# Kernel tuning notes

Measured on AMD Instinct MI355X. Metric: run time of the kernel, lower is better.

## Reference

```python
import jax, jax.numpy as jnp
import numpy as np

NUM_HEADS = 8
NUM_KV_HEADS = 2
HEAD_DIM = 64
EPS = 1e-6
ROPE_BASE = 10000.0


def rmsnorm(x, w):
    # x: (..., head_dim)
    var = jnp.mean(x * x, axis=-1, keepdims=True)
    return x * jax.lax.rsqrt(var + EPS) * w


def apply_rope(x):
    # x: (B, L, nH, hd); positions along L, standard rotate-half RoPE
    B, L, nH, hd = x.shape
    inv_freq = 1.0 / (ROPE_BASE ** (jnp.arange(0, hd, 2, dtype=jnp.float32) / hd))  # (hd/2,)
    ang = jnp.arange(L, dtype=jnp.float32)[:, None] * inv_freq[None, :]  # (L, hd/2)
    cos = jnp.concatenate([jnp.cos(ang), jnp.cos(ang)], axis=-1)[None, :, None, :]  # (1,L,1,hd)
    sin = jnp.concatenate([jnp.sin(ang), jnp.sin(ang)], axis=-1)[None, :, None, :]
    x1, x2 = jnp.split(x, 2, axis=-1)
    rot = jnp.concatenate([-x2, x1], axis=-1)
    return x * cos + rot * sin


def setup_inputs() -> dict:
    key = jax.random.key(0)
    ks = jax.random.split(key, 6)
    width = 512
    x = jax.random.normal(ks[0], (1, 16, 16, 16, width), dtype=jnp.float32)
    s = 1.0 / np.sqrt(width)
    Wq = jax.random.normal(ks[1], (width, width), dtype=jnp.float32) * s
    Wk = jax.random.normal(ks[2], (NUM_KV_HEADS * HEAD_DIM, width), dtype=jnp.float32) * s
    Wv = jax.random.normal(ks[3], (NUM_KV_HEADS * HEAD_DIM, width), dtype=jnp.float32) * s
    Wo = jax.random.normal(ks[4], (width, width), dtype=jnp.float32) * s
    q_norm_w = jnp.ones((HEAD_DIM,), dtype=jnp.float32)
    k_norm_w = jnp.ones((HEAD_DIM,), dtype=jnp.float32)
    return {"x": x, "Wq": Wq, "Wk": Wk, "Wv": Wv,
            "q_norm_w": q_norm_w, "k_norm_w": k_norm_w, "Wo": Wo}


def reference(x, Wq, Wk, Wv, q_norm_w, k_norm_w, Wo):
    B, H, W, D, C = x.shape
    L = H * W * D
    xf = x.reshape(B, L, C)
    q = (xf @ Wq.T).reshape(B, L, NUM_HEADS, HEAD_DIM)
    k = (xf @ Wk.T).reshape(B, L, NUM_KV_HEADS, HEAD_DIM)
    v = (xf @ Wv.T).reshape(B, L, NUM_KV_HEADS, HEAD_DIM)
    q = apply_rope(rmsnorm(q, q_norm_w))
    k = apply_rope(rmsnorm(k, k_norm_w))
    # (B, heads, L, hd)
    q = q.transpose(0, 2, 1, 3)
    k = k.transpose(0, 2, 1, 3)
    v = v.transpose(0, 2, 1, 3)
    repeats = NUM_HEADS // NUM_KV_HEADS
    if repeats > 1:
        k = jnp.repeat(k, repeats, axis=1)
        v = jnp.repeat(v, repeats, axis=1)
    scale = 1.0 / np.sqrt(HEAD_DIM)
    scores = jnp.einsum('bhqd,bhkd->bhqk', q, k) * scale
    attn = jax.nn.softmax(scores, axis=-1)
    out = jnp.einsum('bhqk,bhkd->bhqd', attn, v)
    out = out.transpose(0, 2, 1, 3).reshape(B, H, W, D, C)
    return out @ Wo.T
```

## Files before the change

kernel.cpp:

```cpp
#include <hip/hip_runtime.h>
#include <hip/hip_bf16.h>
#include <math.h>

#define L_SEQ 4096
#define CDIM  512
#define NH    8
#define NKV   2
#define HD    64
#define EPS   1e-6f
#define QSCALE 0.18033688011f

using short8 = __attribute__((ext_vector_type(8))) short;
using f32x4  = __attribute__((ext_vector_type(4))) float;
using f32x16 = __attribute__((ext_vector_type(16))) float;
typedef unsigned short ushort_t;

__device__ __forceinline__ ushort_t f2bf(float f) {
    union { float f; unsigned u; } c; c.f = f;
    unsigned r = c.u + 0x7FFF + ((c.u >> 16) & 1);
    return (ushort_t)(r >> 16);
}
__device__ __forceinline__ float bf2f(ushort_t u) {
    union { unsigned u; float f; } c; c.u = ((unsigned)u) << 16;
    return c.f;
}

#define GLOAD_LDS16(g, l)                                                  \
    __builtin_amdgcn_global_load_lds(                                      \
        (const __attribute__((address_space(1))) unsigned int*)(g),        \
        (__attribute__((address_space(3))) unsigned int*)(l), 16, 0, 0)

__device__ __forceinline__ short8 lds_read8(const char* p) {
    return *reinterpret_cast<const short8*>(__builtin_assume_aligned(p, 16));
}

__device__ __forceinline__ unsigned pk_bf16(float lo, float hi) {
    const __hip_bfloat162 h2 = __float22bfloat162_rn(make_float2(lo, hi));
    unsigned w; __builtin_memcpy(&w, &h2, 4);
    return w;
}

__global__ __launch_bounds__(256) void cvt_bf16(const float* __restrict__ x,
                                                const float* __restrict__ wq,
                                                const float* __restrict__ wk,
                                                const float* __restrict__ wv,
                                                const float* __restrict__ wo,
                                                ushort_t* __restrict__ xb,
                                                ushort_t* __restrict__ wqb,
                                                ushort_t* __restrict__ wkb,
                                                ushort_t* __restrict__ wvb,
                                                ushort_t* __restrict__ wob) {
    const size_t i = ((size_t)blockIdx.x * 256 + threadIdx.x) << 2;
    const float* s; ushort_t* d; size_t o;
    if (i < 2097152)      { s = x;  d = xb;  o = i; }
    else if (i < 2359296) { s = wq; d = wqb; o = i - 2097152; }
    else if (i < 2424832) { s = wk; d = wkb; o = i - 2359296; }
    else if (i < 2490368) { s = wv; d = wvb; o = i - 2424832; }
    else                  { s = wo; d = wob; o = i - 2490368; }
    const float4 v = *reinterpret_cast<const float4*>(s + o);
    ushort_t r[4] = { f2bf(v.x), f2bf(v.y), f2bf(v.z), f2bf(v.w) };
    *reinterpret_cast<uint2*>(d + o) = *reinterpret_cast<const uint2*>(r);
}

__global__ __launch_bounds__(256) void qkv_gemm(const ushort_t* __restrict__ xb,
                                                const ushort_t* __restrict__ wqb,
                                                const ushort_t* __restrict__ wkb,
                                                const ushort_t* __restrict__ wvb,
                                                const float* __restrict__ qnw,
                                                const float* __restrict__ knw,
                                                ushort_t* __restrict__ qbuf,
                                                ushort_t* __restrict__ kbuf,
                                                ushort_t* __restrict__ vtb) {
    __shared__ char smem[32768];
    short (*As)[4096] = (short(*)[4096])smem;
    short (*Bs)[4096] = (short(*)[4096])(smem + 16384);
    float (*F)[65]    = (float(*)[65])smem;

    const int bid = blockIdx.x;
    int which, m0, n0;
    const ushort_t *A, *B;
    if (bid < 512)      { which = 0; A = xb;  B = wqb; m0 = (bid >> 3) * 64; n0 = (bid & 7) * 64; }
    else if (bid < 640) { which = 1; A = xb;  B = wkb; const int i = bid - 512; m0 = (i >> 1) * 64; n0 = (i & 1) * 64; }
    else                { which = 2; A = wvb; B = xb;  const int i = bid - 640; m0 = (i & 1) * 64; n0 = (i >> 1) * 64; }

    const int tid = threadIdx.x;
    const int w = tid >> 6, lane = tid & 63;
    const int g = lane >> 4, r16 = lane & 15;
    const int wr = w >> 1, wc = w & 1;
    const int r7sw = (r16 & 7) << 4;

    const int lrow = lane >> 3;
    const int swzb = ((lane & 7) ^ lrow) << 4;
    const int c0 = w * 2, c1 = w * 2 + 1;
    const size_t rowK2 = (size_t)CDIM * 2;

    const char* agA = (const char*)A + (size_t)(m0 + c0 * 8 + lrow) * rowK2 + swzb;
    const char* agB = agA + 8 * rowK2;
    const char* bgA = (const char*)B + (size_t)(n0 + c0 * 8 + lrow) * rowK2 + swzb;
    const char* bgB = bgA + 8 * rowK2;

    GLOAD_LDS16(agA, (char*)As[0] + c0 * 1024);
    GLOAD_LDS16(agB, (char*)As[0] + c1 * 1024);
    GLOAD_LDS16(bgA, (char*)Bs[0] + c0 * 1024);
    GLOAD_LDS16(bgB, (char*)Bs[0] + c1 * 1024);
    __syncthreads();

    f32x4 acc[2][2] = {};
    int cur = 0;
    for (int it = 0; it < CDIM / 64; ++it) {
        if (it + 1 < CDIM / 64) {
            const size_t ko = (size_t)(it + 1) * 128;
            char* ad = (char*)As[cur ^ 1];
            char* bd = (char*)Bs[cur ^ 1];
            GLOAD_LDS16(agA + ko, ad + c0 * 1024);
            GLOAD_LDS16(agB + ko, ad + c1 * 1024);
            GLOAD_LDS16(bgA + ko, bd + c0 * 1024);
            GLOAD_LDS16(bgB + ko, bd + c1 * 1024);
        }
        const char* at = (const char*)As[cur];
        const char* bt = (const char*)Bs[cur];

        short8 af[2][2], bfr[2][2];
#pragma unroll
        for (int t = 0; t < 2; ++t)
#pragma unroll
            for (int ks = 0; ks < 2; ++ks) {
                af[t][ks]  = lds_read8(at + (wr * 32 + t * 16 + r16) * 128
                                          + ((ks * 64 + g * 16) ^ r7sw));
                bfr[t][ks] = lds_read8(bt + (wc * 32 + t * 16 + r16) * 128
                                          + ((ks * 64 + g * 16) ^ r7sw));
            }
        __builtin_amdgcn_s_setprio(1);
#pragma unroll
        for (int tm = 0; tm < 2; ++tm)
#pragma unroll
            for (int tn = 0; tn < 2; ++tn)
#pragma unroll
                for (int ks = 0; ks < 2; ++ks)
                    acc[tm][tn] = __builtin_amdgcn_mfma_f32_16x16x32_bf16(
                        af[tm][ks], bfr[tn][ks], acc[tm][tn], 0, 0, 0);
        __builtin_amdgcn_s_setprio(0);

        __syncthreads();
        cur ^= 1;
    }

    if (which == 2) {
#pragma unroll
        for (int tm = 0; tm < 2; ++tm)
#pragma unroll
            for (int tn = 0; tn < 2; ++tn)
#pragma unroll
                for (int jj = 0; jj < 4; ++jj) {
                    const int row = m0 + wr * 32 + tm * 16 + g * 4 + jj;
                    const int col = n0 + wc * 32 + tn * 16 + r16;
                    vtb[(size_t)row * L_SEQ + col] = f2bf(acc[tm][tn][jj]);
                }
        return;
    }

#pragma unroll
    for (int tm = 0; tm < 2; ++tm)
#pragma unroll
        for (int tn = 0; tn < 2; ++tn)
#pragma unroll
            for (int jj = 0; jj < 4; ++jj)
                F[wr * 32 + tm * 16 + g * 4 + jj][wc * 32 + tn * 16 + r16] = acc[tm][tn][jj];
    __syncthreads();

    const float wv_ = (which == 0 ? qnw : knw)[lane];
    const int i31 = lane & 31;
    const float invf = exp2f((float)i31 * -0.41524101186f);
    ushort_t* dst = (which == 0) ? qbuf : kbuf;
    const int ncols = (which == 0) ? (NH * HD) : (NKV * HD);

    for (int rr = 0; rr < 16; ++rr) {
        const int rl = w * 16 + rr;
        const int pos = m0 + rl;
        float x = F[rl][lane];
        float ss = x * x;
#pragma unroll
        for (int off = 32; off; off >>= 1) ss += __shfl_xor(ss, off);
        float xn = x * rsqrtf(ss * (1.0f / 64.0f) + EPS) * wv_;
        float xp = __shfl_xor(xn, 32);
        float sn, cs;
        sincosf((float)pos * invf, &sn, &cs);
        float out = (lane < 32) ? (xn * cs - xp * sn) : (xn * cs + xp * sn);
        if (which == 0) out *= QSCALE;
        dst[(size_t)pos * ncols + n0 + lane] = f2bf(out);
    }
}

template<bool OUT_BF16>
__global__ __launch_bounds__(256) void gemm_bf16_nt(const ushort_t* __restrict__ A,
                                                    const ushort_t* __restrict__ B,
                                                    void* __restrict__ Cv,
                                                    int M, int N, int K) {
    __shared__ short As[2][4096];
    __shared__ short Bs[2][4096];

    const int tid = threadIdx.x;
    const int w = tid >> 6, lane = tid & 63;
    const int g = lane >> 4, r16 = lane & 15;
    const int wr = w >> 1, wc = w & 1;
    const int m0 = blockIdx.y * 64, n0 = blockIdx.x * 64;
    const int r7sw = (r16 & 7) << 4;

    const int lrow = lane >> 3;
    const int swzb = ((lane & 7) ^ lrow) << 4;
    const int c0 = w * 2, c1 = w * 2 + 1;
    const size_t rowK2 = (size_t)K * 2;

    const char* agA = (const char*)A + (size_t)(m0 + c0 * 8 + lrow) * rowK2 + swzb;
    const char* agB = agA + 8 * rowK2;
    const char* bgA = (const char*)B + (size_t)(n0 + c0 * 8 + lrow) * rowK2 + swzb;
    const char* bgB = bgA + 8 * rowK2;

    GLOAD_LDS16(agA, (char*)As[0] + c0 * 1024);
    GLOAD_LDS16(agB, (char*)As[0] + c1 * 1024);
    GLOAD_LDS16(bgA, (char*)Bs[0] + c0 * 1024);
    GLOAD_LDS16(bgB, (char*)Bs[0] + c1 * 1024);
    __syncthreads();

    f32x4 acc[2][2] = {};
    const int NKIT = K >> 6;
    int cur = 0;
    for (int it = 0; it < NKIT; ++it) {
        if (it + 1 < NKIT) {
            const size_t ko = (size_t)(it + 1) * 128;
            char* ad = (char*)As[cur ^ 1];
            char* bd = (char*)Bs[cur ^ 1];
            GLOAD_LDS16(agA + ko, ad + c0 * 1024);
            GLOAD_LDS16(agB + ko, ad + c1 * 1024);
            GLOAD_LDS16(bgA + ko, bd + c0 * 1024);
            GLOAD_LDS16(bgB + ko, bd + c1 * 1024);
        }
        const char* at = (const char*)As[cur];
        const char* bt = (const char*)Bs[cur];

        short8 af[2][2], bfr[2][2];
#pragma unroll
        for (int t = 0; t < 2; ++t)
#pragma unroll
            for (int ks = 0; ks < 2; ++ks) {
                af[t][ks]  = lds_read8(at + (wr * 32 + t * 16 + r16) * 128
                                          + ((ks * 64 + g * 16) ^ r7sw));
                bfr[t][ks] = lds_read8(bt + (wc * 32 + t * 16 + r16) * 128
                                          + ((ks * 64 + g * 16) ^ r7sw));
            }
        __builtin_amdgcn_s_setprio(1);
#pragma unroll
        for (int tm = 0; tm < 2; ++tm)
#pragma unroll
            for (int tn = 0; tn < 2; ++tn)
#pragma unroll
                for (int ks = 0; ks < 2; ++ks)
                    acc[tm][tn] = __builtin_amdgcn_mfma_f32_16x16x32_bf16(
                        af[tm][ks], bfr[tn][ks], acc[tm][tn], 0, 0, 0);
        __builtin_amdgcn_s_setprio(0);

        __syncthreads();
        cur ^= 1;
    }

#pragma unroll
    for (int tm = 0; tm < 2; ++tm)
#pragma unroll
        for (int tn = 0; tn < 2; ++tn)
#pragma unroll
            for (int jj = 0; jj < 4; ++jj) {
                const int row = m0 + wr * 32 + tm * 16 + g * 4 + jj;
                const int col = n0 + wc * 32 + tn * 16 + r16;
                if (OUT_BF16)
                    ((ushort_t*)Cv)[(size_t)row * N + col] = f2bf(acc[tm][tn][jj]);
                else
                    ((float*)Cv)[(size_t)row * N + col] = acc[tm][tn][jj];
            }
}

__global__ __launch_bounds__(256, 2) void attn_mfma(const ushort_t* __restrict__ qb,
                                                    const ushort_t* __restrict__ kb,
                                                    const ushort_t* __restrict__ vtb,
                                                    ushort_t* __restrict__ opart,
                                                    float* __restrict__ lpart) {
    __shared__ short Ks[2][4096];
    __shared__ short Vs[2][4096];

    const int tid = threadIdx.x;
    const int w = tid >> 6, lane = tid & 63;
    const int l31 = lane & 31, hf = lane >> 5;
    const int h = blockIdx.y, hkv = h >> 2;
    const int s = blockIdx.z;
    const int kvspan = L_SEQ / gridDim.z;
    const int kvb = s * kvspan;
    const int qw = blockIdx.x * 256 + w * 64;
    const int swz = (lane & 7) << 4;

    const int lrow = lane >> 3;
    const int swzb = ((lane & 7) ^ lrow) << 4;
    const int c0 = w * 2, c1 = w * 2 + 1;

    const char* kgA = (const char*)kb + (size_t)(kvb + c0 * 8 + lrow) * (NKV * HD * 2)
                      + hkv * (HD * 2) + swzb;
    const char* kgB = kgA + 8 * (NKV * HD * 2);
    const char* vgA = (const char*)vtb + (size_t)(hkv * HD + c0 * 8 + lrow) * (L_SEQ * 2)
                      + (size_t)kvb * 2 + swzb;
    const char* vgB = vgA + 8 * (size_t)(L_SEQ * 2);

    short8 qf0[4], qf1[4];
#pragma unroll
    for (int ks = 0; ks < 4; ++ks) {
        qf0[ks] = *reinterpret_cast<const short8*>(
            &qb[(size_t)(qw + l31) * CDIM + h * HD + ks * 16 + hf * 8]);
        qf1[ks] = *reinterpret_cast<const short8*>(
            &qb[(size_t)(qw + 32 + l31) * CDIM + h * HD + ks * 16 + hf * 8]);
    }

    GLOAD_LDS16(kgA, (char*)Ks[0] + c0 * 1024);
    GLOAD_LDS16(kgB, (char*)Ks[0] + c1 * 1024);
    GLOAD_LDS16(vgA, (char*)Vs[0] + c0 * 1024);
    GLOAD_LDS16(vgB, (char*)Vs[0] + c1 * 1024);
    __syncthreads();

    f32x16 oacc0[2] = {}, oacc1[2] = {};
    float ls0[2] = {}, ls1[2] = {};

    int cur = 0;
    const int nit = kvspan >> 6;
    for (int it = 0; it < nit; ++it) {
        if (it + 1 < nit) {
            const size_t ko = (size_t)(it + 1) * 64 * (NKV * HD * 2);
            const size_t vo = (size_t)(it + 1) * 128;
            char* kd = (char*)Ks[cur ^ 1];
            char* vd = (char*)Vs[cur ^ 1];
            GLOAD_LDS16(kgA + ko, kd + c0 * 1024);
            GLOAD_LDS16(kgB + ko, kd + c1 * 1024);
            GLOAD_LDS16(vgA + vo, vd + c0 * 1024);
            GLOAD_LDS16(vgB + vo, vd + c1 * 1024);
        }

        const char* kt = (const char*)Ks[cur];
        const char* vt = (const char*)Vs[cur];

#pragma unroll
        for (int sub = 0; sub < 2; ++sub) {
            f32x16 s0 = {}, s1 = {};
            __builtin_amdgcn_s_setprio(1);
#pragma unroll
            for (int ks = 0; ks < 4; ++ks) {
                const short8 kfr = lds_read8(
                    kt + (sub * 32 + l31) * 128 + ((ks * 32 + hf * 16) ^ swz));
                s0 = __builtin_amdgcn_mfma_f32_32x32x16_bf16(kfr, qf0[ks], s0, 0, 0, 0);
                s1 = __builtin_amdgcn_mfma_f32_32x32x16_bf16(kfr, qf1[ks], s1, 0, 0, 0);
            }
            __builtin_amdgcn_s_setprio(0);

            unsigned pk0[8], pk1[8];
#pragma unroll
            for (int r2 = 0; r2 < 8; ++r2) {
                const float x0 = exp2f(s0[2 * r2]), y0 = exp2f(s0[2 * r2 + 1]);
                const float x1 = exp2f(s1[2 * r2]), y1 = exp2f(s1[2 * r2 + 1]);
                ls0[r2 & 1] += x0 + y0;
                ls1[r2 & 1] += x1 + y1;
                pk0[r2] = pk_bf16(x0, y0);
                pk1[r2] = pk_bf16(x1, y1);
            }

            short8 pf0[2], pf1[2];
#pragma unroll
            for (int kkl = 0; kkl < 2; ++kkl) {
                auto a0 = __builtin_amdgcn_permlane32_swap(pk0[kkl * 4 + 0], pk0[kkl * 4 + 2], false, false);
                auto a1 = __builtin_amdgcn_permlane32_swap(pk0[kkl * 4 + 1], pk0[kkl * 4 + 3], false, false);
                auto b0 = __builtin_amdgcn_permlane32_swap(pk1[kkl * 4 + 0], pk1[kkl * 4 + 2], false, false);
                auto b1 = __builtin_amdgcn_permlane32_swap(pk1[kkl * 4 + 1], pk1[kkl * 4 + 3], false, false);
                union { unsigned u[4]; short8 s8; } u0, u1;
                u0.u[0] = a0[0]; u0.u[1] = a1[0]; u0.u[2] = a0[1]; u0.u[3] = a1[1];
                u1.u[0] = b0[0]; u1.u[1] = b1[0]; u1.u[2] = b0[1]; u1.u[3] = b1[1];
                pf0[kkl] = u0.s8; pf1[kkl] = u1.s8;
            }

            __builtin_amdgcn_s_setprio(1);
#pragma unroll
            for (int n = 0; n < 2; ++n) {
#pragma unroll
                for (int kkl = 0; kkl < 2; ++kkl) {
                    const short8 vf = lds_read8(
                        vt + (n * 32 + l31) * 128 + (((sub * 2 + kkl) * 32 + hf * 16) ^ swz));
                    oacc0[n] = __builtin_amdgcn_mfma_f32_32x32x16_bf16(pf0[kkl], vf, oacc0[n], 0, 0, 0);
                    oacc1[n] = __builtin_amdgcn_mfma_f32_32x32x16_bf16(pf1[kkl], vf, oacc1[n], 0, 0, 0);
                }
            }
            __builtin_amdgcn_s_setprio(0);
        }

        __syncthreads();
        cur ^= 1;
    }

    float lsA = ls0[0] + ls0[1];
    float lsB = ls1[0] + ls1[1];
    lsA += __shfl_xor(lsA, 32);
    lsB += __shfl_xor(lsB, 32);
    ushort_t* op = opart + (size_t)s * L_SEQ * CDIM;
    float* lp = lpart + (size_t)s * L_SEQ * NH;
    if (lane < 32) {
        lp[(size_t)(qw + lane) * NH + h] = lsA;
        lp[(size_t)(qw + 32 + lane) * NH + h] = lsB;
    }
#pragma unroll
    for (int n = 0; n < 2; ++n)
#pragma unroll
        for (int r = 0; r < 16; ++r) {
            const int rr = (r & 3) + 8 * (r >> 2) + 4 * hf;
            op[(size_t)(qw + rr) * CDIM + h * HD + n * 32 + l31] = f2bf(oacc0[n][r]);
            op[(size_t)(qw + 32 + rr) * CDIM + h * HD + n * 32 + l31] = f2bf(oacc1[n][r]);
        }
}

__global__ __launch_bounds__(256) void combine_splits(const ushort_t* __restrict__ opart,
                                                      const float* __restrict__ lpart,
                                                      ushort_t* __restrict__ out,
                                                      int nsplit) {
    const size_t i4 = ((size_t)blockIdx.x * 256 + threadIdx.x) << 2;
    const int row = (int)(i4 >> 9);
    const int h = (int)((i4 & 511) >> 6);
    float l = 0.0f;
    for (int s = 0; s < nsplit; ++s)
        l += lpart[(size_t)s * L_SEQ * NH + (size_t)row * NH + h];
    const float inv = 1.0f / l;

    float acc[4] = {};
    for (int s = 0; s < nsplit; ++s) {
        ushort_t a[4];
        *reinterpret_cast<uint2*>(a) =
            *reinterpret_cast<const uint2*>(opart + (size_t)s * L_SEQ * CDIM + i4);
#pragma unroll
        for (int j = 0; j < 4; ++j) acc[j] += bf2f(a[j]);
    }
    ushort_t r[4];
#pragma unroll
    for (int j = 0; j < 4; ++j) r[j] = f2bf(acc[j] * inv);
    *reinterpret_cast<uint2*>(out + i4) = *reinterpret_cast<const uint2*>(r);
}

extern "C" void kernel_launch(void* const* d_in, const int* in_sizes, int n_in,
                              void* d_out, int out_size, void* d_ws, size_t ws_size,
                              hipStream_t stream) {
    const float* x   = (const float*)d_in[0];
    const float* Wq  = (const float*)d_in[1];
    const float* Wk  = (const float*)d_in[2];
    const float* Wv  = (const float*)d_in[3];
    const float* qnw = (const float*)d_in[4];
    const float* knw = (const float*)d_in[5];
    const float* Wo  = (const float*)d_in[6];
    float* out = (float*)d_out;

    const size_t tail = (size_t)L_SEQ * CDIM * 2
                      + (size_t)L_SEQ * NKV * HD * 2 * 2
                      + (size_t)CDIM * CDIM * 2 * 2
                      + (size_t)NKV * HD * CDIM * 2 * 2
                      + (size_t)8 * L_SEQ * NH * 4;
    const size_t need8 = (size_t)8 * L_SEQ * CDIM * 2 + tail;
    const int nsplit = (ws_size >= need8) ? 8 : 4;

    char* p = (char*)d_ws;
    ushort_t* opart = (ushort_t*)p;
    ushort_t* xb    = opart;
    ushort_t* abuf  = opart;
    char* q = p + (size_t)nsplit * L_SEQ * CDIM * 2;
    ushort_t* qbuf = (ushort_t*)q;
    ushort_t* kbuf = qbuf + (size_t)L_SEQ * CDIM;
    ushort_t* vtb  = kbuf + (size_t)L_SEQ * NKV * HD;
    ushort_t* wqb  = vtb  + (size_t)L_SEQ * NKV * HD;
    ushort_t* wkb  = wqb  + (size_t)CDIM * CDIM;
    ushort_t* wvb  = wkb  + (size_t)NKV * HD * CDIM;
    ushort_t* wob  = wvb  + (size_t)NKV * HD * CDIM;
    float*    lpart = (float*)(wob + (size_t)CDIM * CDIM);

    const dim3 blk(256);

    cvt_bf16<<<dim3(2688), blk, 0, stream>>>(x, Wq, Wk, Wv, Wo, xb, wqb, wkb, wvb, wob);

    qkv_gemm<<<dim3(768), blk, 0, stream>>>(xb, wqb, wkb, wvb, qnw, knw, qbuf, kbuf, vtb);

    attn_mfma<<<dim3(L_SEQ / 256, NH, nsplit), blk, 0, stream>>>(qbuf, kbuf, vtb, opart, lpart);

    combine_splits<<<dim3((L_SEQ * CDIM) / (256 * 4)), blk, 0, stream>>>(opart, lpart, abuf, nsplit);

    gemm_bf16_nt<false><<<dim3(8, 64), blk, 0, stream>>>(abuf, wob, out, L_SEQ, CDIM, CDIM);
}
```

Measured before the change: 102.5 us.

## Precompute RoPE sin/cos table in convert kernel and fix split count to four

Adds 512 extra blocks to the conversion kernel that build a sin/cos table for RoPE (4096 positions x 32 frequencies). The QKV epilogue reads this table instead of calling sincosf per element. It also drops the workspace-size check and hardcodes the attention split count to 4, where it could previously be 8. That changes how work is spread across the attention grid and adds table reads in place of transcendental math.

```diff
diff --git a/kernel.cpp b/kernel.cpp
--- a/kernel.cpp
+++ b/kernel.cpp
@@ -9,6 +9,7 @@
 #define HD    64
 #define EPS   1e-6f
 #define QSCALE 0.18033688011f
+#define NSPLIT 4
 
 using short8 = __attribute__((ext_vector_type(8))) short;
 using f32x4  = __attribute__((ext_vector_type(4))) float;
@@ -49,8 +50,19 @@
                                                 ushort_t* __restrict__ wqb,
                                                 ushort_t* __restrict__ wkb,
                                                 ushort_t* __restrict__ wvb,
-                                                ushort_t* __restrict__ wob) {
-    const size_t i = ((size_t)blockIdx.x * 256 + threadIdx.x) << 2;
+                                                ushort_t* __restrict__ wob,
+                                                float2* __restrict__ rope_tab) {
+    const size_t tidg = (size_t)blockIdx.x * 256 + threadIdx.x;
+    if (blockIdx.x >= 2688) {
+        const int idx = (int)(tidg - (size_t)2688 * 256);
+        const int pos = idx >> 5, i = idx & 31;
+        const float invf = exp2f((float)i * -0.41524101186f);
+        float sn, cs;
+        sincosf((float)pos * invf, &sn, &cs);
+        rope_tab[idx] = make_float2(sn, cs);
+        return;
+    }
+    const size_t i = tidg << 2;
     const float* s; ushort_t* d; size_t o;
     if (i < 2097152)      { s = x;  d = xb;  o = i; }
     else if (i < 2359296) { s = wq; d = wqb; o = i - 2097152; }
@@ -68,6 +80,7 @@
                                                 const ushort_t* __restrict__ wvb,
                                                 const float* __restrict__ qnw,
                                                 const float* __restrict__ knw,
+                                                const float2* __restrict__ rope_tab,
                                                 ushort_t* __restrict__ qbuf,
                                                 ushort_t* __restrict__ kbuf,
                                                 ushort_t* __restrict__ vtb) {
@@ -170,7 +183,6 @@
 
     const float wv_ = (which == 0 ? qnw : knw)[lane];
     const int i31 = lane & 31;
-    const float invf = exp2f((float)i31 * -0.41524101186f);
     ushort_t* dst = (which == 0) ? qbuf : kbuf;
     const int ncols = (which == 0) ? (NH * HD) : (NKV * HD);
 
@@ -183,9 +195,8 @@
         for (int off = 32; off; off >>= 1) ss += __shfl_xor(ss, off);
         float xn = x * rsqrtf(ss * (1.0f / 64.0f) + EPS) * wv_;
         float xp = __shfl_xor(xn, 32);
-        float sn, cs;
-        sincosf((float)pos * invf, &sn, &cs);
-        float out = (lane < 32) ? (xn * cs - xp * sn) : (xn * cs + xp * sn);
+        const float2 sc = rope_tab[pos * 32 + i31];
+        float out = (lane < 32) ? (xn * sc.y - xp * sc.x) : (xn * sc.y + xp * sc.x);
         if (which == 0) out *= QSCALE;
         dst[(size_t)pos * ncols + n0 + lane] = f2bf(out);
     }
@@ -455,19 +466,11 @@
     const float* Wo  = (const float*)d_in[6];
     float* out = (float*)d_out;
 
-    const size_t tail = (size_t)L_SEQ * CDIM * 2
-                      + (size_t)L_SEQ * NKV * HD * 2 * 2
-                      + (size_t)CDIM * CDIM * 2 * 2
-                      + (size_t)NKV * HD * CDIM * 2 * 2
-                      + (size_t)8 * L_SEQ * NH * 4;
-    const size_t need8 = (size_t)8 * L_SEQ * CDIM * 2 + tail;
-    const int nsplit = (ws_size >= need8) ? 8 : 4;
-
     char* p = (char*)d_ws;
     ushort_t* opart = (ushort_t*)p;
     ushort_t* xb    = opart;
     ushort_t* abuf  = opart;
-    char* q = p + (size_t)nsplit * L_SEQ * CDIM * 2;
+    char* q = p + (size_t)NSPLIT * L_SEQ * CDIM * 2;
     ushort_t* qbuf = (ushort_t*)q;
     ushort_t* kbuf = qbuf + (size_t)L_SEQ * CDIM;
     ushort_t* vtb  = kbuf + (size_t)L_SEQ * NKV * HD;
@@ -476,16 +479,19 @@
     ushort_t* wvb  = wkb  + (size_t)NKV * HD * CDIM;
     ushort_t* wob  = wvb  + (size_t)NKV * HD * CDIM;
     float*    lpart = (float*)(wob + (size_t)CDIM * CDIM);
+    float2*   rope_tab = (float2*)(lpart + (size_t)NSPLIT * L_SEQ * NH);
 
     const dim3 blk(256);
 
-    cvt_bf16<<<dim3(2688), blk, 0, stream>>>(x, Wq, Wk, Wv, Wo, xb, wqb, wkb, wvb, wob);
-
-    qkv_gemm<<<dim3(768), blk, 0, stream>>>(xb, wqb, wkb, wvb, qnw, knw, qbuf, kbuf, vtb);
-
-    attn_mfma<<<dim3(L_SEQ / 256, NH, nsplit), blk, 0, stream>>>(qbuf, kbuf, vtb, opart, lpart);
-
-    combine_splits<<<dim3((L_SEQ * CDIM) / (256 * 4)), blk, 0, stream>>>(opart, lpart, abuf, nsplit);
+    cvt_bf16<<<dim3(3200), blk, 0, stream>>>(x, Wq, Wk, Wv, Wo,
+                                             xb, wqb, wkb, wvb, wob, rope_tab);
+
+    qkv_gemm<<<dim3(768), blk, 0, stream>>>(xb, wqb, wkb, wvb, qnw, knw,
+                                            rope_tab, qbuf, kbuf, vtb);
+
+    attn_mfma<<<dim3(L_SEQ / 256, NH, NSPLIT), blk, 0, stream>>>(qbuf, kbuf, vtb, opart, lpart);
+
+    combine_splits<<<dim3((L_SEQ * CDIM) / (256 * 4)), blk, 0, stream>>>(opart, lpart, abuf, NSPLIT);
 
     gemm_bf16_nt<false><<<dim3(8, 64), blk, 0, stream>>>(abuf, wob, out, L_SEQ, CDIM, CDIM);
 }
```

After: 95.82 us. 6.5% less time.
